# Performance work log

Measured on AMD Instinct MI355X. Metric: run time of the kernel, lower is better.

The kernel has to match this reference:

```python
import jax, jax.numpy as jnp
import numpy as np

MIDC = 128
HEADS = 4
HEADC = MIDC // HEADS
EPS = 1e-5


def _layernorm(x, w, b):
    # Faithful to the custom torch LayerNorm: unbiased std (ddof=1) and (std + eps) in denominator.
    mean = jnp.mean(x, axis=-1, keepdims=True)
    std = jnp.std(x, axis=-1, keepdims=True, ddof=1)
    return w * ((x - mean) / (std + EPS)) + b


def setup_inputs() -> dict:
    key = jax.random.key(0)
    ks = jax.random.split(key, 8)
    B, C, D, H, W = 2, MIDC, 16, 64, 64
    s = 1.0 / np.sqrt(C)
    return {
        "x": jax.random.normal(ks[0], (B, C, D, H, W), dtype=jnp.float32),
        "qkv_w": jax.random.normal(ks[1], (3 * C, C), dtype=jnp.float32) * s,
        "qkv_b": jnp.zeros((3 * C,), dtype=jnp.float32),
        "o1_w": jax.random.normal(ks[2], (C, C), dtype=jnp.float32) * s,
        "o1_b": jnp.zeros((C,), dtype=jnp.float32),
        "o2_w": jax.random.normal(ks[3], (C, C), dtype=jnp.float32) * s,
        "o2_b": jnp.zeros((C,), dtype=jnp.float32),
        "kln_w": jnp.ones((HEADS, 1, HEADC), dtype=jnp.float32),
        "kln_b": jnp.zeros((HEADS, 1, HEADC), dtype=jnp.float32),
        "vln_w": jnp.ones((HEADS, 1, HEADC), dtype=jnp.float32),
        "vln_b": jnp.zeros((HEADS, 1, HEADC), dtype=jnp.float32),
    }


def reference(x, qkv_w, qkv_b, o1_w, o1_b, o2_w, o2_b, kln_w, kln_b, vln_w, vln_b):
    B, C, D, H, W = x.shape
    heads, headc = HEADS, HEADC
    bias = x
    # 1x1x1 Conv3d == pointwise linear over channel dim
    qkv = jnp.einsum('bcdhw,oc->bdhwo', x, qkv_w) + qkv_b          # [B,D,H,W,3C]
    qkv = qkv.reshape(B * D, H * W, heads, 3 * headc)
    qkv = qkv.transpose(0, 2, 1, 3)                                 # [BD,heads,HW,3hc]
    q, k, v = jnp.split(qkv, 3, axis=-1)                            # each [BD,heads,HW,hc]
    k = _layernorm(k, kln_w, kln_b)
    v = _layernorm(v, vln_w, vln_b)
    # linear attention: (K^T V) then Q (K^T V)
    kv = jnp.einsum('bhnc,bhnd->bhcd', k, v) / (H * W)              # [BD,heads,hc,hc]
    v = jnp.einsum('bhnc,bhcd->bhnd', q, kv)                        # [BD,heads,HW,hc]
    v = v.transpose(0, 2, 1, 3).reshape(B, D, H, W, C)
    ret = v.transpose(0, 4, 1, 2, 3) + bias                         # [B,C,D,H,W]
    h = jnp.einsum('bcdhw,oc->bodhw', ret, o1_w) + o1_b[None, :, None, None, None]
    h = jax.nn.gelu(h, approximate=False)
    out = jnp.einsum('bcdhw,oc->bodhw', h, o2_w) + o2_b[None, :, None, None, None]
    return out + bias
```

## Files before the change

### kernel.cpp

```cpp
#include <hip/hip_runtime.h>
#include <cmath>

typedef float  f32x4  __attribute__((ext_vector_type(4)));
typedef __bf16 bf16x8 __attribute__((ext_vector_type(8)));
typedef __bf16 bf16x4 __attribute__((ext_vector_type(4)));
typedef __bf16 bf16x2 __attribute__((ext_vector_type(2)));

#define MFMA16(acc, a, b) (acc) = __builtin_amdgcn_mfma_f32_16x16x32_bf16((a), (b), (acc), 0, 0, 0)


__device__ __forceinline__ int swz(int row, int colByte){ return row*256 + (colByte ^ ((row & 7) << 4)); }
__device__ __forceinline__ int swzP(int row, int colByte){ return row*128 + (colByte ^ ((row & 7) << 4)); }

__device__ __forceinline__ void loadx(float* sx, const float* __restrict__ xb, int t){
  int p = t & 63, cg = t >> 6;
  const float* col = xb + p;
  #pragma unroll
  for (int i = 0; i < 4; ++i)
    #pragma unroll
    for (int j = 0; j < 8; ++j)
      sx[i*8 + j] = col[(cg*8 + i*32 + j) * 65536];
}
__device__ __forceinline__ void writex(const float* sx, char* ldsX, int t){
  int p = t & 63, cg = t >> 6;
  #pragma unroll
  for (int i = 0; i < 4; ++i){
    bf16x8 u;
    #pragma unroll
    for (int j = 0; j < 8; ++j) u[j] = (__bf16)sx[i*8 + j];
    *(bf16x8*)(ldsX + swz(p, cg*16 + i*64)) = u;
  }
}

__global__ __launch_bounds__(256) void wprep(const float* __restrict__ qkv_w,
                                             const float* __restrict__ o1w,
                                             const float* __restrict__ o2w,
                                             __bf16* __restrict__ w16){
  int e = (blockIdx.x * 256 + threadIdx.x) * 4;
  const float* src; int off;
  if (e < 49152)      { src = qkv_w; off = e; }
  else if (e < 65536) { src = o1w;   off = e - 49152; }
  else                { src = o2w;   off = e - 65536; }
  f32x4 v = *(const f32x4*)(src + off);
  bf16x4 o;
  #pragma unroll
  for (int r = 0; r < 4; ++r) o[r] = (__bf16)v[r];
  *(bf16x4*)(w16 + e) = o;
}

__global__ __launch_bounds__(256) void k1_kv(
    const float* __restrict__ x, const __bf16* __restrict__ w16, const float* __restrict__ qkv_b,
    const float* __restrict__ klw, const float* __restrict__ klb,
    const float* __restrict__ vlw, const float* __restrict__ vlb,
    __bf16* __restrict__ part){
  __shared__ char ldsX[16384];
  __shared__ char ksS[4][4096];
  int t = threadIdx.x, lane = t & 63, w = t >> 6, l15 = lane & 15, l4 = lane >> 4;
  int bx = blockIdx.x, bd = bx >> 6, b = bd >> 4, d = bd & 15;
  const float* xb = x + (size_t)b*8388608 + d*4096 + (bx & 63)*64;
  char* ks = ksS[w];
  char* vs = ldsX + w * 4096;

  {
    float sx[32];
    loadx(sx, xb, t);
    writex(sx, ldsX, t);
  }
  __syncthreads();

  bf16x4 pv0[4], pv1[4];
  #pragma unroll
  for (int ph = 0; ph < 2; ++ph){
    int po = 96*w + 32 + 32*ph;
    f32x4 acc[2][4] = {};
    #pragma unroll
    for (int kf = 0; kf < 4; ++kf){
      bf16x8 a0 = *(const bf16x8*)(w16 + (po + l15)*128 + kf*32 + l4*8);
      bf16x8 a1 = *(const bf16x8*)(w16 + (po + 16 + l15)*128 + kf*32 + l4*8);
      bf16x8 bn0 = *(const bf16x8*)(ldsX + swz(l15,      kf*64 + l4*16));
      bf16x8 bn1 = *(const bf16x8*)(ldsX + swz(16 + l15, kf*64 + l4*16));
      bf16x8 bn2 = *(const bf16x8*)(ldsX + swz(32 + l15, kf*64 + l4*16));
      bf16x8 bn3 = *(const bf16x8*)(ldsX + swz(48 + l15, kf*64 + l4*16));
      MFMA16(acc[0][0], a0, bn0); MFMA16(acc[0][1], a0, bn1);
      MFMA16(acc[0][2], a0, bn2); MFMA16(acc[0][3], a0, bn3);
      MFMA16(acc[1][0], a1, bn0); MFMA16(acc[1][1], a1, bn1);
      MFMA16(acc[1][2], a1, bn2); MFMA16(acc[1][3], a1, bn3);
    }
    const float* lwp = (ph ? vlw : klw) + 32*w;
    const float* lbp = (ph ? vlb : klb) + 32*w;
    f32x4 b0  = *(const f32x4*)(qkv_b + po + l4*4);
    f32x4 b1  = *(const f32x4*)(qkv_b + po + 16 + l4*4);
    f32x4 lw0 = *(const f32x4*)(lwp + l4*4), lw1 = *(const f32x4*)(lwp + 16 + l4*4);
    f32x4 lb0 = *(const f32x4*)(lbp + l4*4), lb1 = *(const f32x4*)(lbp + 16 + l4*4);
    #pragma unroll
    for (int n = 0; n < 4; ++n){
      f32x4 v0 = acc[0][n] + b0;
      f32x4 v1 = acc[1][n] + b1;
      float s1 = v0[0]+v0[1]+v0[2]+v0[3] + v1[0]+v1[1]+v1[2]+v1[3];
      float s2 = v0[0]*v0[0]+v0[1]*v0[1]+v0[2]*v0[2]+v0[3]*v0[3]
               + v1[0]*v1[0]+v1[1]*v1[1]+v1[2]*v1[2]+v1[3]*v1[3];
      s1 += __shfl_xor(s1, 16); s2 += __shfl_xor(s2, 16);
      s1 += __shfl_xor(s1, 32); s2 += __shfl_xor(s2, 32);
      float m   = s1 * (1.f/32.f);
      float var = fmaxf((s2 - 32.f*m*m) * (1.f/31.f), 0.f);
      float inv = 1.f / (sqrtf(var) + 1e-5f);
      v0 = (v0 - m) * inv * lw0 + lb0;
      v1 = (v1 - m) * inv * lw1 + lb1;
      if (ph == 0){
        int pB = (16*n + l15) * 2;
        #pragma unroll
        for (int r = 0; r < 4; ++r){
          *(__bf16*)(ks + swzP(l4*4 + r, pB))      = (__bf16)v0[r];
          *(__bf16*)(ks + swzP(16 + l4*4 + r, pB)) = (__bf16)v1[r];
        }
      } else {
        #pragma unroll
        for (int r = 0; r < 4; ++r){ pv0[n][r] = (__bf16)v0[r]; pv1[n][r] = (__bf16)v1[r]; }
      }
    }
  }
  __syncthreads();
  #pragma unroll
  for (int n = 0; n < 4; ++n){
    int pB = (16*n + l15) * 2;
    #pragma unroll
    for (int r = 0; r < 4; ++r){
      *(__bf16*)(vs + swzP(l4*4 + r, pB))      = pv0[n][r];
      *(__bf16*)(vs + swzP(16 + l4*4 + r, pB)) = pv1[n][r];
    }
  }
  f32x4 kv[2][2] = {};
  #pragma unroll
  for (int kf = 0; kf < 2; ++kf){
    bf16x8 av0 = *(const bf16x8*)(vs + swzP(l15,      kf*64 + l4*16));
    bf16x8 av1 = *(const bf16x8*)(vs + swzP(16 + l15, kf*64 + l4*16));
    bf16x8 bk0 = *(const bf16x8*)(ks + swzP(l15,      kf*64 + l4*16));
    bf16x8 bk1 = *(const bf16x8*)(ks + swzP(16 + l15, kf*64 + l4*16));
    MFMA16(kv[0][0], av0, bk0); MFMA16(kv[0][1], av0, bk1);
    MFMA16(kv[1][0], av1, bk0); MFMA16(kv[1][1], av1, bk1);
  }

  __bf16* pb = part + (size_t)bx*4096 + w*1024;
  #pragma unroll
  for (int m = 0; m < 2; ++m)
    #pragma unroll
    for (int n = 0; n < 2; ++n)
      #pragma unroll
      for (int r = 0; r < 4; ++r)
        pb[(16*m + l4*4 + r)*32 + 16*n + l15] = (__bf16)kv[m][n][r];
}

__global__ __launch_bounds__(256) void k15_reduce(const __bf16* __restrict__ part,
                                                  float* __restrict__ kvt){
  int bx = blockIdx.x, t = threadIdx.x;
  int bd = bx >> 3, seg = bx & 7;
  int e = seg * 512 + t * 2;
  float s0 = 0.f, s1 = 0.f;
  #pragma unroll
  for (int sub = 0; sub < 64; ++sub){
    bf16x2 p = *(const bf16x2*)(part + (size_t)(bd * 64 + sub) * 4096 + e);
    s0 += (float)p[0]; s1 += (float)p[1];
  }
  kvt[bd * 4096 + e]     = s0 * (1.f / 4096.f);
  kvt[bd * 4096 + e + 1] = s1 * (1.f / 4096.f);
}

__global__ __launch_bounds__(256, 5) void k2_main(
    const float* __restrict__ x, const __bf16* __restrict__ w16, const float* __restrict__ qkv_b,
    const float* __restrict__ o1b, const float* __restrict__ o2b,
    const float* __restrict__ kvt, float* __restrict__ out){
  __shared__ char lx[16384];
  __shared__ char wk[16384];
  int t = threadIdx.x, lane = t & 63, w = t >> 6, l15 = lane & 15, l4 = lane >> 4;
  int bx = blockIdx.x, bd = bx >> 6, b = bd >> 4, d = bd & 15;
  size_t gofs = (size_t)b*8388608 + d*4096 + (bx & 63)*64;
  const float* xb = x + gofs;
  float* ob = out + gofs;
  const __bf16* w1 = w16 + 49152;
  const __bf16* w2 = w16 + 65536;
  int oo = 32 * w;

  float sx[32];
  loadx(sx, xb, t);
  const float* kvh = kvt + ((size_t)bd*4 + w)*1024;
  f32x4 ql0 = *(const f32x4*)(kvh + l15*32 + l4*8);
  f32x4 qh0 = *(const f32x4*)(kvh + l15*32 + l4*8 + 4);
  f32x4 ql1 = *(const f32x4*)(kvh + (16 + l15)*32 + l4*8);
  f32x4 qh1 = *(const f32x4*)(kvh + (16 + l15)*32 + l4*8 + 4);
  writex(sx, lx, t);
  bf16x8 ka0, ka1;
  #pragma unroll
  for (int j = 0; j < 4; ++j){
    ka0[j] = (__bf16)ql0[j]; ka0[j+4] = (__bf16)qh0[j];
    ka1[j] = (__bf16)ql1[j]; ka1[j+4] = (__bf16)qh1[j];
  }
  __syncthreads();

  {
    bf16x8 A0[4], A1[4];
    #pragma unroll
    for (int kf = 0; kf < 4; ++kf){
      A0[kf] = *(const bf16x8*)(w16 + (96*w + l15)*128 + kf*32 + l4*8);
      A1[kf] = *(const bf16x8*)(w16 + (96*w + 16 + l15)*128 + kf*32 + l4*8);
    }
    f32x4 acc[2][4] = {};
    #pragma unroll
    for (int kf = 0; kf < 4; ++kf){
      bf16x8 bn0 = *(const bf16x8*)(lx + swz(l15,      kf*64 + l4*16));
      bf16x8 bn1 = *(const bf16x8*)(lx + swz(16 + l15, kf*64 + l4*16));
      bf16x8 bn2 = *(const bf16x8*)(lx + swz(32 + l15, kf*64 + l4*16));
      bf16x8 bn3 = *(const bf16x8*)(lx + swz(48 + l15, kf*64 + l4*16));
      MFMA16(acc[0][0], A0[kf], bn0); MFMA16(acc[0][1], A0[kf], bn1);
      MFMA16(acc[0][2], A0[kf], bn2); MFMA16(acc[0][3], A0[kf], bn3);
      MFMA16(acc[1][0], A1[kf], bn0); MFMA16(acc[1][1], A1[kf], bn1);
      MFMA16(acc[1][2], A1[kf], bn2); MFMA16(acc[1][3], A1[kf], bn3);
    }
    #pragma unroll
    for (int m = 0; m < 2; ++m){
      f32x4 qb = *(const f32x4*)(qkv_b + 96*w + 16*m + l4*4);
      int cB = (oo + 16*m + l4*4) * 2;
      #pragma unroll
      for (int n = 0; n < 4; ++n){
        bf16x4 pk;
        #pragma unroll
        for (int r = 0; r < 4; ++r) pk[r] = (__bf16)(acc[m][n][r] + qb[r]);
        *(bf16x4*)(wk + swz(16*n + l15, cB)) = pk;
      }
    }
  }
  {
    f32x4 acc[2][4] = {};
    #pragma unroll
    for (int n = 0; n < 4; ++n){
      bf16x8 bq = *(const bf16x8*)(wk + swz(16*n + l15, oo*2 + l4*16));
      MFMA16(acc[0][n], ka0, bq);
      MFMA16(acc[1][n], ka1, bq);
    }
    #pragma unroll
    for (int m = 0; m < 2; ++m){
      int cB = (oo + 16*m + l4*4) * 2;
      #pragma unroll
      for (int n = 0; n < 4; ++n){
        bf16x4 xv = *(const bf16x4*)(lx + swz(16*n + l15, cB));
        bf16x4 pk;
        #pragma unroll
        for (int r = 0; r < 4; ++r) pk[r] = (__bf16)(acc[m][n][r] + (float)xv[r]);
        *(bf16x4*)(wk + swz(16*n + l15, cB)) = pk;
      }
    }
  }
  __syncthreads();

  {
    bf16x8 A0[4], A1[4];
    #pragma unroll
    for (int kf = 0; kf < 4; ++kf){
      A0[kf] = *(const bf16x8*)(w1 + (oo + l15)*128 + kf*32 + l4*8);
      A1[kf] = *(const bf16x8*)(w1 + (oo + 16 + l15)*128 + kf*32 + l4*8);
    }
    f32x4 acc1[2][4] = {};
    #pragma unroll
    for (int kf = 0; kf < 4; ++kf){
      bf16x8 bn0 = *(const bf16x8*)(wk + swz(l15,      kf*64 + l4*16));
      bf16x8 bn1 = *(const bf16x8*)(wk + swz(16 + l15, kf*64 + l4*16));
      bf16x8 bn2 = *(const bf16x8*)(wk + swz(32 + l15, kf*64 + l4*16));
      bf16x8 bn3 = *(const bf16x8*)(wk + swz(48 + l15, kf*64 + l4*16));
      MFMA16(acc1[0][0], A0[kf], bn0); MFMA16(acc1[0][1], A0[kf], bn1);
      MFMA16(acc1[0][2], A0[kf], bn2); MFMA16(acc1[0][3], A0[kf], bn3);
      MFMA16(acc1[1][0], A1[kf], bn0); MFMA16(acc1[1][1], A1[kf], bn1);
      MFMA16(acc1[1][2], A1[kf], bn2); MFMA16(acc1[1][3], A1[kf], bn3);
    }
    bf16x4 hk[2][4];
    #pragma unroll
    for (int m = 0; m < 2; ++m){
      f32x4 bb = *(const f32x4*)(o1b + oo + 16*m + l4*4);
      #pragma unroll
      for (int n = 0; n < 4; ++n)
        #pragma unroll
        for (int r = 0; r < 4; ++r){
          float v = acc1[m][n][r] + bb[r];
          float z = v * (1.5957691216f + 0.0713548164f * v * v);
          hk[m][n][r] = (__bf16)(v / (1.f + __expf(-z)));
        }
    }
    __syncthreads();
    #pragma unroll
    for (int m = 0; m < 2; ++m){
      int cB = (oo + 16*m + l4*4) * 2;
      #pragma unroll
      for (int n = 0; n < 4; ++n)
        *(bf16x4*)(wk + swz(16*n + l15, cB)) = hk[m][n];
    }
  }
  __syncthreads();

  {
    bf16x8 A0[4], A1[4];
    #pragma unroll
    for (int kf = 0; kf < 4; ++kf){
      A0[kf] = *(const bf16x8*)(w2 + (oo + l15)*128 + kf*32 + l4*8);
      A1[kf] = *(const bf16x8*)(w2 + (oo + 16 + l15)*128 + kf*32 + l4*8);
    }
    f32x4 acc2[2][4] = {};
    #pragma unroll
    for (int kf = 0; kf < 4; ++kf){
      bf16x8 bn0 = *(const bf16x8*)(wk + swz(l15,      kf*64 + l4*16));
      bf16x8 bn1 = *(const bf16x8*)(wk + swz(16 + l15, kf*64 + l4*16));
      bf16x8 bn2 = *(const bf16x8*)(wk + swz(32 + l15, kf*64 + l4*16));
      bf16x8 bn3 = *(const bf16x8*)(wk + swz(48 + l15, kf*64 + l4*16));
      MFMA16(acc2[0][0], A0[kf], bn0); MFMA16(acc2[0][1], A0[kf], bn1);
      MFMA16(acc2[0][2], A0[kf], bn2); MFMA16(acc2[0][3], A0[kf], bn3);
      MFMA16(acc2[1][0], A1[kf], bn0); MFMA16(acc2[1][1], A1[kf], bn1);
      MFMA16(acc2[1][2], A1[kf], bn2); MFMA16(acc2[1][3], A1[kf], bn3);
    }
    #pragma unroll
    for (int m = 0; m < 2; ++m){
      int c0 = oo + 16*m + l4*4;
      f32x4 bb = *(const f32x4*)(o2b + c0);
      #pragma unroll
      for (int n = 0; n < 4; ++n){
        bf16x4 xv = *(const bf16x4*)(lx + swz(16*n + l15, c0*2));
        #pragma unroll
        for (int r = 0; r < 4; ++r)
          ob[(size_t)(c0 + r)*65536 + 16*n + l15] = acc2[m][n][r] + bb[r] + (float)xv[r];
      }
    }
  }
}

extern "C" void kernel_launch(void* const* d_in, const int* in_sizes, int n_in,
                              void* d_out, int out_size, void* d_ws, size_t ws_size,
                              hipStream_t stream){
  const float* x     = (const float*)d_in[0];
  const float* qkv_w = (const float*)d_in[1];
  const float* qkv_b = (const float*)d_in[2];
  const float* o1w   = (const float*)d_in[3];
  const float* o1b   = (const float*)d_in[4];
  const float* o2w   = (const float*)d_in[5];
  const float* o2b   = (const float*)d_in[6];
  const float* klw   = (const float*)d_in[7];
  const float* klb   = (const float*)d_in[8];
  const float* vlw   = (const float*)d_in[9];
  const float* vlb   = (const float*)d_in[10];

  __bf16* part = (__bf16*)d_out;
  float*  kvt  = (float*)d_ws;
  __bf16* w16  = (__bf16*)((char*)d_ws + 524288);

  wprep<<<80, 256, 0, stream>>>(qkv_w, o1w, o2w, w16);
  k1_kv<<<2048, 256, 0, stream>>>(x, w16, qkv_b, klw, klb, vlw, vlb, part);
  k15_reduce<<<256, 256, 0, stream>>>(part, kvt);
  k2_main<<<2048, 256, 0, stream>>>(x, w16, qkv_b, o1b, o2b, kvt, (float*)d_out);
}
```

Measured before the change: 92.00 us.

## Repartition k2_main so each wave owns 16 pixels through QKV, attention and o1

Moves the per-wave split in the fused main kernel from output-channel slices to pixel slices for the q projection, the Q·KV product and the first output conv. Each wave keeps its own 16-pixel activations in a private 4 KB LDS region, which removes two block-wide barriers and the shared staging between stages. Each wave now loads all weight rows from global memory for its MFMAs, where before it loaded only its channel slice. The occupancy hint of 5 in launch_bounds is also dropped, which changes register allocation and could raise register pressure.

```diff
diff --git a/kernel.cpp b/kernel.cpp
--- a/kernel.cpp
+++ b/kernel.cpp
@@ -165,7 +165,7 @@
   kvt[bd * 4096 + e + 1] = s1 * (1.f / 4096.f);
 }
 
-__global__ __launch_bounds__(256, 5) void k2_main(
+__global__ __launch_bounds__(256) void k2_main(
     const float* __restrict__ x, const __bf16* __restrict__ w16, const float* __restrict__ qkv_b,
     const float* __restrict__ o1b, const float* __restrict__ o2b,
     const float* __restrict__ kvt, float* __restrict__ out){
@@ -178,140 +178,113 @@
   float* ob = out + gofs;
   const __bf16* w1 = w16 + 49152;
   const __bf16* w2 = w16 + 65536;
-  int oo = 32 * w;
-
-  float sx[32];
-  loadx(sx, xb, t);
-  const float* kvh = kvt + ((size_t)bd*4 + w)*1024;
-  f32x4 ql0 = *(const f32x4*)(kvh + l15*32 + l4*8);
-  f32x4 qh0 = *(const f32x4*)(kvh + l15*32 + l4*8 + 4);
-  f32x4 ql1 = *(const f32x4*)(kvh + (16 + l15)*32 + l4*8);
-  f32x4 qh1 = *(const f32x4*)(kvh + (16 + l15)*32 + l4*8 + 4);
-  writex(sx, lx, t);
-  bf16x8 ka0, ka1;
-  #pragma unroll
-  for (int j = 0; j < 4; ++j){
-    ka0[j] = (__bf16)ql0[j]; ka0[j+4] = (__bf16)qh0[j];
-    ka1[j] = (__bf16)ql1[j]; ka1[j+4] = (__bf16)qh1[j];
+  char* s = wk + w * 4096;
+
+  {
+    float sx[32];
+    loadx(sx, xb, t);
+    writex(sx, lx, t);
   }
   __syncthreads();
 
   {
-    bf16x8 A0[4], A1[4];
+    f32x4 acc[8] = {};
     #pragma unroll
     for (int kf = 0; kf < 4; ++kf){
-      A0[kf] = *(const bf16x8*)(w16 + (96*w + l15)*128 + kf*32 + l4*8);
-      A1[kf] = *(const bf16x8*)(w16 + (96*w + 16 + l15)*128 + kf*32 + l4*8);
-    }
-    f32x4 acc[2][4] = {};
+      bf16x8 bq = *(const bf16x8*)(lx + swz(w*16 + l15, kf*64 + l4*16));
+      #pragma unroll
+      for (int m = 0; m < 8; ++m){
+        bf16x8 a = *(const bf16x8*)(w16 + (96*(m>>1) + (m&1)*16 + l15)*128 + kf*32 + l4*8);
+        MFMA16(acc[m], a, bq);
+      }
+    }
+    #pragma unroll
+    for (int m = 0; m < 8; ++m){
+      f32x4 qb = *(const f32x4*)(qkv_b + 96*(m>>1) + (m&1)*16 + l4*4);
+      int ch0 = 32*(m>>1) + (m&1)*16 + l4*4;
+      bf16x4 pk;
+      #pragma unroll
+      for (int r = 0; r < 4; ++r) pk[r] = (__bf16)(acc[m][r] + qb[r]);
+      *(bf16x4*)(s + swz(l15, ch0*2)) = pk;
+    }
+  }
+
+  {
+    const float* kvb = kvt + (size_t)bd*4096;
+    #pragma unroll
+    for (int h = 0; h < 4; ++h){
+      const float* kvh = kvb + h*1024;
+      f32x4 ql0 = *(const f32x4*)(kvh + l15*32 + l4*8);
+      f32x4 qh0 = *(const f32x4*)(kvh + l15*32 + l4*8 + 4);
+      f32x4 ql1 = *(const f32x4*)(kvh + (16 + l15)*32 + l4*8);
+      f32x4 qh1 = *(const f32x4*)(kvh + (16 + l15)*32 + l4*8 + 4);
+      bf16x8 ka0, ka1;
+      #pragma unroll
+      for (int j = 0; j < 4; ++j){
+        ka0[j] = (__bf16)ql0[j]; ka0[j+4] = (__bf16)qh0[j];
+        ka1[j] = (__bf16)ql1[j]; ka1[j+4] = (__bf16)qh1[j];
+      }
+      bf16x8 bq = *(const bf16x8*)(s + swz(l15, h*64 + l4*16));
+      f32x4 r0 = {}, r1 = {};
+      MFMA16(r0, ka0, bq);
+      MFMA16(r1, ka1, bq);
+      int ch0 = 32*h + l4*4;
+      bf16x4 xv0 = *(const bf16x4*)(lx + swz(w*16 + l15, ch0*2));
+      bf16x4 xv1 = *(const bf16x4*)(lx + swz(w*16 + l15, (ch0 + 16)*2));
+      bf16x4 p0, p1;
+      #pragma unroll
+      for (int r = 0; r < 4; ++r){
+        p0[r] = (__bf16)(r0[r] + (float)xv0[r]);
+        p1[r] = (__bf16)(r1[r] + (float)xv1[r]);
+      }
+      *(bf16x4*)(s + swz(l15, ch0*2)) = p0;
+      *(bf16x4*)(s + swz(l15, (ch0 + 16)*2)) = p1;
+    }
+  }
+
+  {
+    bf16x8 bn[4];
+    #pragma unroll
+    for (int kf = 0; kf < 4; ++kf)
+      bn[kf] = *(const bf16x8*)(s + swz(l15, kf*64 + l4*16));
+    f32x4 acc[8] = {};
+    #pragma unroll
+    for (int kf = 0; kf < 4; ++kf)
+      #pragma unroll
+      for (int m = 0; m < 8; ++m){
+        bf16x8 a = *(const bf16x8*)(w1 + (16*m + l15)*128 + kf*32 + l4*8);
+        MFMA16(acc[m], a, bn[kf]);
+      }
+    #pragma unroll
+    for (int m = 0; m < 8; ++m){
+      f32x4 bb = *(const f32x4*)(o1b + 16*m + l4*4);
+      bf16x4 pk;
+      #pragma unroll
+      for (int r = 0; r < 4; ++r){
+        float v = acc[m][r] + bb[r];
+        float z = v * (1.5957691216f + 0.0713548164f * v * v);
+        pk[r] = (__bf16)(v / (1.f + __expf(-z)));
+      }
+      *(bf16x4*)(s + swz(l15, (16*m + l4*4)*2)) = pk;
+    }
+  }
+  __syncthreads();
+
+  {
+    int oo = 32 * w;
+    f32x4 acc2[2][4] = {};
     #pragma unroll
     for (int kf = 0; kf < 4; ++kf){
-      bf16x8 bn0 = *(const bf16x8*)(lx + swz(l15,      kf*64 + l4*16));
-      bf16x8 bn1 = *(const bf16x8*)(lx + swz(16 + l15, kf*64 + l4*16));
-      bf16x8 bn2 = *(const bf16x8*)(lx + swz(32 + l15, kf*64 + l4*16));
-      bf16x8 bn3 = *(const bf16x8*)(lx + swz(48 + l15, kf*64 + l4*16));
-      MFMA16(acc[0][0], A0[kf], bn0); MFMA16(acc[0][1], A0[kf], bn1);
-      MFMA16(acc[0][2], A0[kf], bn2); MFMA16(acc[0][3], A0[kf], bn3);
-      MFMA16(acc[1][0], A1[kf], bn0); MFMA16(acc[1][1], A1[kf], bn1);
-      MFMA16(acc[1][2], A1[kf], bn2); MFMA16(acc[1][3], A1[kf], bn3);
-    }
-    #pragma unroll
-    for (int m = 0; m < 2; ++m){
-      f32x4 qb = *(const f32x4*)(qkv_b + 96*w + 16*m + l4*4);
-      int cB = (oo + 16*m + l4*4) * 2;
-      #pragma unroll
-      for (int n = 0; n < 4; ++n){
-        bf16x4 pk;
-        #pragma unroll
-        for (int r = 0; r < 4; ++r) pk[r] = (__bf16)(acc[m][n][r] + qb[r]);
-        *(bf16x4*)(wk + swz(16*n + l15, cB)) = pk;
-      }
-    }
-  }
-  {
-    f32x4 acc[2][4] = {};
-    #pragma unroll
-    for (int n = 0; n < 4; ++n){
-      bf16x8 bq = *(const bf16x8*)(wk + swz(16*n + l15, oo*2 + l4*16));
-      MFMA16(acc[0][n], ka0, bq);
-      MFMA16(acc[1][n], ka1, bq);
-    }
-    #pragma unroll
-    for (int m = 0; m < 2; ++m){
-      int cB = (oo + 16*m + l4*4) * 2;
-      #pragma unroll
-      for (int n = 0; n < 4; ++n){
-        bf16x4 xv = *(const bf16x4*)(lx + swz(16*n + l15, cB));
-        bf16x4 pk;
-        #pragma unroll
-        for (int r = 0; r < 4; ++r) pk[r] = (__bf16)(acc[m][n][r] + (float)xv[r]);
-        *(bf16x4*)(wk + swz(16*n + l15, cB)) = pk;
-      }
-    }
-  }
-  __syncthreads();
-
-  {
-    bf16x8 A0[4], A1[4];
-    #pragma unroll
-    for (int kf = 0; kf < 4; ++kf){
-      A0[kf] = *(const bf16x8*)(w1 + (oo + l15)*128 + kf*32 + l4*8);
-      A1[kf] = *(const bf16x8*)(w1 + (oo + 16 + l15)*128 + kf*32 + l4*8);
-    }
-    f32x4 acc1[2][4] = {};
-    #pragma unroll
-    for (int kf = 0; kf < 4; ++kf){
-      bf16x8 bn0 = *(const bf16x8*)(wk + swz(l15,      kf*64 + l4*16));
-      bf16x8 bn1 = *(const bf16x8*)(wk + swz(16 + l15, kf*64 + l4*16));
-      bf16x8 bn2 = *(const bf16x8*)(wk + swz(32 + l15, kf*64 + l4*16));
-      bf16x8 bn3 = *(const bf16x8*)(wk + swz(48 + l15, kf*64 + l4*16));
-      MFMA16(acc1[0][0], A0[kf], bn0); MFMA16(acc1[0][1], A0[kf], bn1);
-      MFMA16(acc1[0][2], A0[kf], bn2); MFMA16(acc1[0][3], A0[kf], bn3);
-      MFMA16(acc1[1][0], A1[kf], bn0); MFMA16(acc1[1][1], A1[kf], bn1);
-      MFMA16(acc1[1][2], A1[kf], bn2); MFMA16(acc1[1][3], A1[kf], bn3);
-    }
-    bf16x4 hk[2][4];
-    #pragma unroll
-    for (int m = 0; m < 2; ++m){
-      f32x4 bb = *(const f32x4*)(o1b + oo + 16*m + l4*4);
-      #pragma unroll
-      for (int n = 0; n < 4; ++n)
-        #pragma unroll
-        for (int r = 0; r < 4; ++r){
-          float v = acc1[m][n][r] + bb[r];
-          float z = v * (1.5957691216f + 0.0713548164f * v * v);
-          hk[m][n][r] = (__bf16)(v / (1.f + __expf(-z)));
-        }
-    }
-    __syncthreads();
-    #pragma unroll
-    for (int m = 0; m < 2; ++m){
-      int cB = (oo + 16*m + l4*4) * 2;
-      #pragma unroll
-      for (int n = 0; n < 4; ++n)
-        *(bf16x4*)(wk + swz(16*n + l15, cB)) = hk[m][n];
-    }
-  }
-  __syncthreads();
-
-  {
-    bf16x8 A0[4], A1[4];
-    #pragma unroll
-    for (int kf = 0; kf < 4; ++kf){
-      A0[kf] = *(const bf16x8*)(w2 + (oo + l15)*128 + kf*32 + l4*8);
-      A1[kf] = *(const bf16x8*)(w2 + (oo + 16 + l15)*128 + kf*32 + l4*8);
-    }
-    f32x4 acc2[2][4] = {};
-    #pragma unroll
-    for (int kf = 0; kf < 4; ++kf){
-      bf16x8 bn0 = *(const bf16x8*)(wk + swz(l15,      kf*64 + l4*16));
-      bf16x8 bn1 = *(const bf16x8*)(wk + swz(16 + l15, kf*64 + l4*16));
-      bf16x8 bn2 = *(const bf16x8*)(wk + swz(32 + l15, kf*64 + l4*16));
-      bf16x8 bn3 = *(const bf16x8*)(wk + swz(48 + l15, kf*64 + l4*16));
-      MFMA16(acc2[0][0], A0[kf], bn0); MFMA16(acc2[0][1], A0[kf], bn1);
-      MFMA16(acc2[0][2], A0[kf], bn2); MFMA16(acc2[0][3], A0[kf], bn3);
-      MFMA16(acc2[1][0], A1[kf], bn0); MFMA16(acc2[1][1], A1[kf], bn1);
-      MFMA16(acc2[1][2], A1[kf], bn2); MFMA16(acc2[1][3], A1[kf], bn3);
+      bf16x8 a0 = *(const bf16x8*)(w2 + (oo + l15)*128 + kf*32 + l4*8);
+      bf16x8 a1 = *(const bf16x8*)(w2 + (oo + 16 + l15)*128 + kf*32 + l4*8);
+      bf16x8 bn0 = *(const bf16x8*)(wk +        swz(l15, kf*64 + l4*16));
+      bf16x8 bn1 = *(const bf16x8*)(wk + 4096 + swz(l15, kf*64 + l4*16));
+      bf16x8 bn2 = *(const bf16x8*)(wk + 8192 + swz(l15, kf*64 + l4*16));
+      bf16x8 bn3 = *(const bf16x8*)(wk + 12288 + swz(l15, kf*64 + l4*16));
+      MFMA16(acc2[0][0], a0, bn0); MFMA16(acc2[0][1], a0, bn1);
+      MFMA16(acc2[0][2], a0, bn2); MFMA16(acc2[0][3], a0, bn3);
+      MFMA16(acc2[1][0], a1, bn0); MFMA16(acc2[1][1], a1, bn1);
+      MFMA16(acc2[1][2], a1, bn2); MFMA16(acc2[1][3], a1, bn3);
     }
     #pragma unroll
     for (int m = 0; m < 2; ++m){
```

After: 140.0 us. +52.1%, slower.

## Alias shared buffers in main kernel and split k/v projection into halves

Applied to the files above, without the earlier changes.

The main kernel now uses a single 16KB LDS buffer instead of two. The residual x tile is kept in registers, and an extra barrier lets the Q projection overwrite the x tile in place. The W2 fragments are loaded inside the k-loop rather than preloaded, and the launch-bounds occupancy hint is dropped. In the first kernel, the K/V projection plus layernorm is split into two half-width passes to shrink the accumulator footprint. Together these aim to cut LDS and register pressure so more blocks fit per CU, at the cost of an extra synchronization and more register-held residual data.

```diff
diff --git a/kernel.cpp b/kernel.cpp
--- a/kernel.cpp
+++ b/kernel.cpp
@@ -72,50 +72,50 @@
   #pragma unroll
   for (int ph = 0; ph < 2; ++ph){
     int po = 96*w + 32 + 32*ph;
-    f32x4 acc[2][4] = {};
-    #pragma unroll
-    for (int kf = 0; kf < 4; ++kf){
-      bf16x8 a0 = *(const bf16x8*)(w16 + (po + l15)*128 + kf*32 + l4*8);
-      bf16x8 a1 = *(const bf16x8*)(w16 + (po + 16 + l15)*128 + kf*32 + l4*8);
-      bf16x8 bn0 = *(const bf16x8*)(ldsX + swz(l15,      kf*64 + l4*16));
-      bf16x8 bn1 = *(const bf16x8*)(ldsX + swz(16 + l15, kf*64 + l4*16));
-      bf16x8 bn2 = *(const bf16x8*)(ldsX + swz(32 + l15, kf*64 + l4*16));
-      bf16x8 bn3 = *(const bf16x8*)(ldsX + swz(48 + l15, kf*64 + l4*16));
-      MFMA16(acc[0][0], a0, bn0); MFMA16(acc[0][1], a0, bn1);
-      MFMA16(acc[0][2], a0, bn2); MFMA16(acc[0][3], a0, bn3);
-      MFMA16(acc[1][0], a1, bn0); MFMA16(acc[1][1], a1, bn1);
-      MFMA16(acc[1][2], a1, bn2); MFMA16(acc[1][3], a1, bn3);
-    }
-    const float* lwp = (ph ? vlw : klw) + 32*w;
-    const float* lbp = (ph ? vlb : klb) + 32*w;
-    f32x4 b0  = *(const f32x4*)(qkv_b + po + l4*4);
-    f32x4 b1  = *(const f32x4*)(qkv_b + po + 16 + l4*4);
-    f32x4 lw0 = *(const f32x4*)(lwp + l4*4), lw1 = *(const f32x4*)(lwp + 16 + l4*4);
-    f32x4 lb0 = *(const f32x4*)(lbp + l4*4), lb1 = *(const f32x4*)(lbp + 16 + l4*4);
-    #pragma unroll
-    for (int n = 0; n < 4; ++n){
-      f32x4 v0 = acc[0][n] + b0;
-      f32x4 v1 = acc[1][n] + b1;
-      float s1 = v0[0]+v0[1]+v0[2]+v0[3] + v1[0]+v1[1]+v1[2]+v1[3];
-      float s2 = v0[0]*v0[0]+v0[1]*v0[1]+v0[2]*v0[2]+v0[3]*v0[3]
-               + v1[0]*v1[0]+v1[1]*v1[1]+v1[2]*v1[2]+v1[3]*v1[3];
-      s1 += __shfl_xor(s1, 16); s2 += __shfl_xor(s2, 16);
-      s1 += __shfl_xor(s1, 32); s2 += __shfl_xor(s2, 32);
-      float m   = s1 * (1.f/32.f);
-      float var = fmaxf((s2 - 32.f*m*m) * (1.f/31.f), 0.f);
-      float inv = 1.f / (sqrtf(var) + 1e-5f);
-      v0 = (v0 - m) * inv * lw0 + lb0;
-      v1 = (v1 - m) * inv * lw1 + lb1;
-      if (ph == 0){
-        int pB = (16*n + l15) * 2;
-        #pragma unroll
-        for (int r = 0; r < 4; ++r){
-          *(__bf16*)(ks + swzP(l4*4 + r, pB))      = (__bf16)v0[r];
-          *(__bf16*)(ks + swzP(16 + l4*4 + r, pB)) = (__bf16)v1[r];
+    #pragma unroll
+    for (int nh = 0; nh < 2; ++nh){
+      f32x4 acc[2][2] = {};
+      #pragma unroll
+      for (int kf = 0; kf < 4; ++kf){
+        bf16x8 a0 = *(const bf16x8*)(w16 + (po + l15)*128 + kf*32 + l4*8);
+        bf16x8 a1 = *(const bf16x8*)(w16 + (po + 16 + l15)*128 + kf*32 + l4*8);
+        bf16x8 bn0 = *(const bf16x8*)(ldsX + swz(32*nh + l15,      kf*64 + l4*16));
+        bf16x8 bn1 = *(const bf16x8*)(ldsX + swz(32*nh + 16 + l15, kf*64 + l4*16));
+        MFMA16(acc[0][0], a0, bn0); MFMA16(acc[0][1], a0, bn1);
+        MFMA16(acc[1][0], a1, bn0); MFMA16(acc[1][1], a1, bn1);
+      }
+      const float* lwp = (ph ? vlw : klw) + 32*w;
+      const float* lbp = (ph ? vlb : klb) + 32*w;
+      f32x4 b0  = *(const f32x4*)(qkv_b + po + l4*4);
+      f32x4 b1  = *(const f32x4*)(qkv_b + po + 16 + l4*4);
+      f32x4 lw0 = *(const f32x4*)(lwp + l4*4), lw1 = *(const f32x4*)(lwp + 16 + l4*4);
+      f32x4 lb0 = *(const f32x4*)(lbp + l4*4), lb1 = *(const f32x4*)(lbp + 16 + l4*4);
+      #pragma unroll
+      for (int nn = 0; nn < 2; ++nn){
+        int n = 2*nh + nn;
+        f32x4 v0 = acc[0][nn] + b0;
+        f32x4 v1 = acc[1][nn] + b1;
+        float s1 = v0[0]+v0[1]+v0[2]+v0[3] + v1[0]+v1[1]+v1[2]+v1[3];
+        float s2 = v0[0]*v0[0]+v0[1]*v0[1]+v0[2]*v0[2]+v0[3]*v0[3]
+                 + v1[0]*v1[0]+v1[1]*v1[1]+v1[2]*v1[2]+v1[3]*v1[3];
+        s1 += __shfl_xor(s1, 16); s2 += __shfl_xor(s2, 16);
+        s1 += __shfl_xor(s1, 32); s2 += __shfl_xor(s2, 32);
+        float m   = s1 * (1.f/32.f);
+        float var = fmaxf((s2 - 32.f*m*m) * (1.f/31.f), 0.f);
+        float inv = 1.f / (sqrtf(var) + 1e-5f);
+        v0 = (v0 - m) * inv * lw0 + lb0;
+        v1 = (v1 - m) * inv * lw1 + lb1;
+        if (ph == 0){
+          int pB = (16*n + l15) * 2;
+          #pragma unroll
+          for (int r = 0; r < 4; ++r){
+            *(__bf16*)(ks + swzP(l4*4 + r, pB))      = (__bf16)v0[r];
+            *(__bf16*)(ks + swzP(16 + l4*4 + r, pB)) = (__bf16)v1[r];
+          }
+        } else {
+          #pragma unroll
+          for (int r = 0; r < 4; ++r){ pv0[n][r] = (__bf16)v0[r]; pv1[n][r] = (__bf16)v1[r]; }
         }
-      } else {
-        #pragma unroll
-        for (int r = 0; r < 4; ++r){ pv0[n][r] = (__bf16)v0[r]; pv1[n][r] = (__bf16)v1[r]; }
       }
     }
   }
@@ -165,12 +165,11 @@
   kvt[bd * 4096 + e + 1] = s1 * (1.f / 4096.f);
 }
 
-__global__ __launch_bounds__(256, 5) void k2_main(
+__global__ __launch_bounds__(256) void k2_main(
     const float* __restrict__ x, const __bf16* __restrict__ w16, const float* __restrict__ qkv_b,
     const float* __restrict__ o1b, const float* __restrict__ o2b,
     const float* __restrict__ kvt, float* __restrict__ out){
-  __shared__ char lx[16384];
-  __shared__ char wk[16384];
+  __shared__ char L[16384];
   int t = threadIdx.x, lane = t & 63, w = t >> 6, l15 = lane & 15, l4 = lane >> 4;
   int bx = blockIdx.x, bd = bx >> 6, b = bd >> 4, d = bd & 15;
   size_t gofs = (size_t)b*8388608 + d*4096 + (bx & 63)*64;
@@ -180,14 +179,16 @@
   const __bf16* w2 = w16 + 65536;
   int oo = 32 * w;
 
-  float sx[32];
-  loadx(sx, xb, t);
+  {
+    float sx[32];
+    loadx(sx, xb, t);
+    writex(sx, L, t);
+  }
   const float* kvh = kvt + ((size_t)bd*4 + w)*1024;
   f32x4 ql0 = *(const f32x4*)(kvh + l15*32 + l4*8);
   f32x4 qh0 = *(const f32x4*)(kvh + l15*32 + l4*8 + 4);
   f32x4 ql1 = *(const f32x4*)(kvh + (16 + l15)*32 + l4*8);
   f32x4 qh1 = *(const f32x4*)(kvh + (16 + l15)*32 + l4*8 + 4);
-  writex(sx, lx, t);
   bf16x8 ka0, ka1;
   #pragma unroll
   for (int j = 0; j < 4; ++j){
@@ -196,6 +197,14 @@
   }
   __syncthreads();
 
+  bf16x4 xr[2][4];
+  #pragma unroll
+  for (int m = 0; m < 2; ++m)
+    #pragma unroll
+    for (int n = 0; n < 4; ++n)
+      xr[m][n] = *(const bf16x4*)(L + swz(16*n + l15, (oo + 16*m + l4*4)*2));
+
+  bf16x4 qk[2][4];
   {
     bf16x8 A0[4], A1[4];
     #pragma unroll
@@ -206,10 +215,10 @@
     f32x4 acc[2][4] = {};
     #pragma unroll
     for (int kf = 0; kf < 4; ++kf){
-      bf16x8 bn0 = *(const bf16x8*)(lx + swz(l15,      kf*64 + l4*16));
-      bf16x8 bn1 = *(const bf16x8*)(lx + swz(16 + l15, kf*64 + l4*16));
-      bf16x8 bn2 = *(const bf16x8*)(lx + swz(32 + l15, kf*64 + l4*16));
-      bf16x8 bn3 = *(const bf16x8*)(lx + swz(48 + l15, kf*64 + l4*16));
+      bf16x8 bn0 = *(const bf16x8*)(L + swz(l15,      kf*64 + l4*16));
+      bf16x8 bn1 = *(const bf16x8*)(L + swz(16 + l15, kf*64 + l4*16));
+      bf16x8 bn2 = *(const bf16x8*)(L + swz(32 + l15, kf*64 + l4*16));
+      bf16x8 bn3 = *(const bf16x8*)(L + swz(48 + l15, kf*64 + l4*16));
       MFMA16(acc[0][0], A0[kf], bn0); MFMA16(acc[0][1], A0[kf], bn1);
       MFMA16(acc[0][2], A0[kf], bn2); MFMA16(acc[0][3], A0[kf], bn3);
       MFMA16(acc[1][0], A1[kf], bn0); MFMA16(acc[1][1], A1[kf], bn1);
@@ -218,34 +227,38 @@
     #pragma unroll
     for (int m = 0; m < 2; ++m){
       f32x4 qb = *(const f32x4*)(qkv_b + 96*w + 16*m + l4*4);
+      #pragma unroll
+      for (int n = 0; n < 4; ++n)
+        #pragma unroll
+        for (int r = 0; r < 4; ++r) qk[m][n][r] = (__bf16)(acc[m][n][r] + qb[r]);
+    }
+  }
+  __syncthreads();
+
+  #pragma unroll
+  for (int m = 0; m < 2; ++m){
+    int cB = (oo + 16*m + l4*4) * 2;
+    #pragma unroll
+    for (int n = 0; n < 4; ++n)
+      *(bf16x4*)(L + swz(16*n + l15, cB)) = qk[m][n];
+  }
+  {
+    f32x4 acc[2][4] = {};
+    #pragma unroll
+    for (int n = 0; n < 4; ++n){
+      bf16x8 bq = *(const bf16x8*)(L + swz(16*n + l15, oo*2 + l4*16));
+      MFMA16(acc[0][n], ka0, bq);
+      MFMA16(acc[1][n], ka1, bq);
+    }
+    #pragma unroll
+    for (int m = 0; m < 2; ++m){
       int cB = (oo + 16*m + l4*4) * 2;
       #pragma unroll
       for (int n = 0; n < 4; ++n){
         bf16x4 pk;
         #pragma unroll
-        for (int r = 0; r < 4; ++r) pk[r] = (__bf16)(acc[m][n][r] + qb[r]);
-        *(bf16x4*)(wk + swz(16*n + l15, cB)) = pk;
-      }
-    }
-  }
-  {
-    f32x4 acc[2][4] = {};
-    #pragma unroll
-    for (int n = 0; n < 4; ++n){
-      bf16x8 bq = *(const bf16x8*)(wk + swz(16*n + l15, oo*2 + l4*16));
-      MFMA16(acc[0][n], ka0, bq);
-      MFMA16(acc[1][n], ka1, bq);
-    }
-    #pragma unroll
-    for (int m = 0; m < 2; ++m){
-      int cB = (oo + 16*m + l4*4) * 2;
-      #pragma unroll
-      for (int n = 0; n < 4; ++n){
-        bf16x4 xv = *(const bf16x4*)(lx + swz(16*n + l15, cB));
-        bf16x4 pk;
-        #pragma unroll
-        for (int r = 0; r < 4; ++r) pk[r] = (__bf16)(acc[m][n][r] + (float)xv[r]);
-        *(bf16x4*)(wk + swz(16*n + l15, cB)) = pk;
+        for (int r = 0; r < 4; ++r) pk[r] = (__bf16)(acc[m][n][r] + (float)xr[m][n][r]);
+        *(bf16x4*)(L + swz(16*n + l15, cB)) = pk;
       }
     }
   }
@@ -261,10 +274,10 @@
     f32x4 acc1[2][4] = {};
     #pragma unroll
     for (int kf = 0; kf < 4; ++kf){
-      bf16x8 bn0 = *(const bf16x8*)(wk + swz(l15,      kf*64 + l4*16));
-      bf16x8 bn1 = *(const bf16x8*)(wk + swz(16 + l15, kf*64 + l4*16));
-      bf16x8 bn2 = *(const bf16x8*)(wk + swz(32 + l15, kf*64 + l4*16));
-      bf16x8 bn3 = *(const bf16x8*)(wk + swz(48 + l15, kf*64 + l4*16));
+      bf16x8 bn0 = *(const bf16x8*)(L + swz(l15,      kf*64 + l4*16));
+      bf16x8 bn1 = *(const bf16x8*)(L + swz(16 + l15, kf*64 + l4*16));
+      bf16x8 bn2 = *(const bf16x8*)(L + swz(32 + l15, kf*64 + l4*16));
+      bf16x8 bn3 = *(const bf16x8*)(L + swz(48 + l15, kf*64 + l4*16));
       MFMA16(acc1[0][0], A0[kf], bn0); MFMA16(acc1[0][1], A0[kf], bn1);
       MFMA16(acc1[0][2], A0[kf], bn2); MFMA16(acc1[0][3], A0[kf], bn3);
       MFMA16(acc1[1][0], A1[kf], bn0); MFMA16(acc1[1][1], A1[kf], bn1);
@@ -289,41 +302,35 @@
       int cB = (oo + 16*m + l4*4) * 2;
       #pragma unroll
       for (int n = 0; n < 4; ++n)
-        *(bf16x4*)(wk + swz(16*n + l15, cB)) = hk[m][n];
-    }
-  }
-  __syncthreads();
-
-  {
-    bf16x8 A0[4], A1[4];
-    #pragma unroll
-    for (int kf = 0; kf < 4; ++kf){
-      A0[kf] = *(const bf16x8*)(w2 + (oo + l15)*128 + kf*32 + l4*8);
-      A1[kf] = *(const bf16x8*)(w2 + (oo + 16 + l15)*128 + kf*32 + l4*8);
-    }
+        *(bf16x4*)(L + swz(16*n + l15, cB)) = hk[m][n];
+    }
+  }
+  __syncthreads();
+
+  {
     f32x4 acc2[2][4] = {};
     #pragma unroll
     for (int kf = 0; kf < 4; ++kf){
-      bf16x8 bn0 = *(const bf16x8*)(wk + swz(l15,      kf*64 + l4*16));
-      bf16x8 bn1 = *(const bf16x8*)(wk + swz(16 + l15, kf*64 + l4*16));
-      bf16x8 bn2 = *(const bf16x8*)(wk + swz(32 + l15, kf*64 + l4*16));
-      bf16x8 bn3 = *(const bf16x8*)(wk + swz(48 + l15, kf*64 + l4*16));
-      MFMA16(acc2[0][0], A0[kf], bn0); MFMA16(acc2[0][1], A0[kf], bn1);
-      MFMA16(acc2[0][2], A0[kf], bn2); MFMA16(acc2[0][3], A0[kf], bn3);
-      MFMA16(acc2[1][0], A1[kf], bn0); MFMA16(acc2[1][1], A1[kf], bn1);
-      MFMA16(acc2[1][2], A1[kf], bn2); MFMA16(acc2[1][3], A1[kf], bn3);
+      bf16x8 a0 = *(const bf16x8*)(w2 + (oo + l15)*128 + kf*32 + l4*8);
+      bf16x8 a1 = *(const bf16x8*)(w2 + (oo + 16 + l15)*128 + kf*32 + l4*8);
+      bf16x8 bn0 = *(const bf16x8*)(L + swz(l15,      kf*64 + l4*16));
+      bf16x8 bn1 = *(const bf16x8*)(L + swz(16 + l15, kf*64 + l4*16));
+      bf16x8 bn2 = *(const bf16x8*)(L + swz(32 + l15, kf*64 + l4*16));
+      bf16x8 bn3 = *(const bf16x8*)(L + swz(48 + l15, kf*64 + l4*16));
+      MFMA16(acc2[0][0], a0, bn0); MFMA16(acc2[0][1], a0, bn1);
+      MFMA16(acc2[0][2], a0, bn2); MFMA16(acc2[0][3], a0, bn3);
+      MFMA16(acc2[1][0], a1, bn0); MFMA16(acc2[1][1], a1, bn1);
+      MFMA16(acc2[1][2], a1, bn2); MFMA16(acc2[1][3], a1, bn3);
     }
     #pragma unroll
     for (int m = 0; m < 2; ++m){
       int c0 = oo + 16*m + l4*4;
       f32x4 bb = *(const f32x4*)(o2b + c0);
       #pragma unroll
-      for (int n = 0; n < 4; ++n){
-        bf16x4 xv = *(const bf16x4*)(lx + swz(16*n + l15, c0*2));
+      for (int n = 0; n < 4; ++n)
         #pragma unroll
         for (int r = 0; r < 4; ++r)
-          ob[(size_t)(c0 + r)*65536 + 16*n + l15] = acc2[m][n][r] + bb[r] + (float)xv[r];
-      }
+          ob[(size_t)(c0 + r)*65536 + 16*n + l15] = acc2[m][n][r] + bb[r] + (float)xr[m][n][r];
     }
   }
 }
```

New measurement: 99.28 us. 1.08x slower.

## Fold KV matrix and residual into per-slice effective Q weight matrix

Applied to the files above, without the earlier changes.

Replaces the KV reduce kernel with one that also multiplies the reduced per-head KV matrix into the Q projection weights, adds identity for the residual, and computes an effective bias. The main kernel then does a single GEMM with this per-slice effective weight instead of a Q projection, a KV MFMA stage and a residual add. This removes one MFMA stage plus LDS round trips per tile. In exchange it adds a small serial weight-folding kernel and per-slice bf16 weights read from global memory. The launch-bounds occupancy hint of 5 is also dropped. Folding the identity into bf16 weights may change rounding of the residual path.

```diff
diff --git a/kernel.cpp b/kernel.cpp
--- a/kernel.cpp
+++ b/kernel.cpp
@@ -4,7 +4,6 @@
 typedef float  f32x4  __attribute__((ext_vector_type(4)));
 typedef __bf16 bf16x8 __attribute__((ext_vector_type(8)));
 typedef __bf16 bf16x4 __attribute__((ext_vector_type(4)));
-typedef __bf16 bf16x2 __attribute__((ext_vector_type(2)));
 
 #define MFMA16(acc, a, b) (acc) = __builtin_amdgcn_mfma_f32_16x16x32_bf16((a), (b), (acc), 0, 0, 0)
 
@@ -150,25 +149,53 @@
         pb[(16*m + l4*4 + r)*32 + 16*n + l15] = (__bf16)kv[m][n][r];
 }
 
-__global__ __launch_bounds__(256) void k15_reduce(const __bf16* __restrict__ part,
-                                                  float* __restrict__ kvt){
-  int bx = blockIdx.x, t = threadIdx.x;
-  int bd = bx >> 3, seg = bx & 7;
-  int e = seg * 512 + t * 2;
-  float s0 = 0.f, s1 = 0.f;
-  #pragma unroll
-  for (int sub = 0; sub < 64; ++sub){
-    bf16x2 p = *(const bf16x2*)(part + (size_t)(bd * 64 + sub) * 4096 + e);
-    s0 += (float)p[0]; s1 += (float)p[1];
-  }
-  kvt[bd * 4096 + e]     = s0 * (1.f / 4096.f);
-  kvt[bd * 4096 + e + 1] = s1 * (1.f / 4096.f);
-}
-
-__global__ __launch_bounds__(256, 5) void k2_main(
-    const float* __restrict__ x, const __bf16* __restrict__ w16, const float* __restrict__ qkv_b,
+__global__ __launch_bounds__(256) void kweff(
+    const __bf16* __restrict__ part, const __bf16* __restrict__ w16,
+    const float* __restrict__ qkv_b,
+    __bf16* __restrict__ weff, float* __restrict__ beff){
+  __shared__ float kvsh[1024];
+  int t = threadIdx.x, bx = blockIdx.x;
+  int bd = bx >> 2, h = bx & 3;
+
+  {
+    f32x4 s = {0.f, 0.f, 0.f, 0.f};
+    const __bf16* pb = part + (size_t)bd*64*4096 + h*1024 + t*4;
+    for (int sub = 0; sub < 64; ++sub){
+      bf16x4 p = *(const bf16x4*)(pb + (size_t)sub*4096);
+      #pragma unroll
+      for (int r = 0; r < 4; ++r) s[r] += (float)p[r];
+    }
+    #pragma unroll
+    for (int r = 0; r < 4; ++r) kvsh[t*4 + r] = s[r] * (1.f/4096.f);
+  }
+  __syncthreads();
+
+  int j = t & 127, half = t >> 7;
+  float wq[32];
+  #pragma unroll
+  for (int c = 0; c < 32; ++c) wq[c] = (float)w16[(96*h + c)*128 + j];
+  #pragma unroll
+  for (int dq = 0; dq < 16; ++dq){
+    int dd = half*16 + dq;
+    float s = 0.f;
+    #pragma unroll
+    for (int c = 0; c < 32; ++c) s += kvsh[dd*32 + c] * wq[c];
+    if (32*h + dd == j) s += 1.f;
+    weff[(size_t)bd*16384 + (32*h + dd)*128 + j] = (__bf16)s;
+  }
+  if (t < 32){
+    float s = 0.f;
+    #pragma unroll
+    for (int c = 0; c < 32; ++c) s += qkv_b[96*h + c] * kvsh[t*32 + c];
+    beff[bd*128 + 32*h + t] = s;
+  }
+}
+
+__global__ __launch_bounds__(256) void k2_main(
+    const float* __restrict__ x, const __bf16* __restrict__ w16,
+    const __bf16* __restrict__ weff, const float* __restrict__ beff,
     const float* __restrict__ o1b, const float* __restrict__ o2b,
-    const float* __restrict__ kvt, float* __restrict__ out){
+    float* __restrict__ out){
   __shared__ char lx[16384];
   __shared__ char wk[16384];
   int t = threadIdx.x, lane = t & 63, w = t >> 6, l15 = lane & 15, l4 = lane >> 4;
@@ -178,21 +205,13 @@
   float* ob = out + gofs;
   const __bf16* w1 = w16 + 49152;
   const __bf16* w2 = w16 + 65536;
+  const __bf16* we = weff + (size_t)bd*16384;
   int oo = 32 * w;
 
-  float sx[32];
-  loadx(sx, xb, t);
-  const float* kvh = kvt + ((size_t)bd*4 + w)*1024;
-  f32x4 ql0 = *(const f32x4*)(kvh + l15*32 + l4*8);
-  f32x4 qh0 = *(const f32x4*)(kvh + l15*32 + l4*8 + 4);
-  f32x4 ql1 = *(const f32x4*)(kvh + (16 + l15)*32 + l4*8);
-  f32x4 qh1 = *(const f32x4*)(kvh + (16 + l15)*32 + l4*8 + 4);
-  writex(sx, lx, t);
-  bf16x8 ka0, ka1;
-  #pragma unroll
-  for (int j = 0; j < 4; ++j){
-    ka0[j] = (__bf16)ql0[j]; ka0[j+4] = (__bf16)qh0[j];
-    ka1[j] = (__bf16)ql1[j]; ka1[j+4] = (__bf16)qh1[j];
+  {
+    float sx[32];
+    loadx(sx, xb, t);
+    writex(sx, lx, t);
   }
   __syncthreads();
 
@@ -200,8 +219,8 @@
     bf16x8 A0[4], A1[4];
     #pragma unroll
     for (int kf = 0; kf < 4; ++kf){
-      A0[kf] = *(const bf16x8*)(w16 + (96*w + l15)*128 + kf*32 + l4*8);
-      A1[kf] = *(const bf16x8*)(w16 + (96*w + 16 + l15)*128 + kf*32 + l4*8);
+      A0[kf] = *(const bf16x8*)(we + (oo + l15)*128 + kf*32 + l4*8);
+      A1[kf] = *(const bf16x8*)(we + (oo + 16 + l15)*128 + kf*32 + l4*8);
     }
     f32x4 acc[2][4] = {};
     #pragma unroll
@@ -217,34 +236,13 @@
     }
     #pragma unroll
     for (int m = 0; m < 2; ++m){
-      f32x4 qb = *(const f32x4*)(qkv_b + 96*w + 16*m + l4*4);
+      f32x4 bb = *(const f32x4*)(beff + bd*128 + oo + 16*m + l4*4);
       int cB = (oo + 16*m + l4*4) * 2;
       #pragma unroll
       for (int n = 0; n < 4; ++n){
         bf16x4 pk;
         #pragma unroll
-        for (int r = 0; r < 4; ++r) pk[r] = (__bf16)(acc[m][n][r] + qb[r]);
-        *(bf16x4*)(wk + swz(16*n + l15, cB)) = pk;
-      }
-    }
-  }
-  {
-    f32x4 acc[2][4] = {};
-    #pragma unroll
-    for (int n = 0; n < 4; ++n){
-      bf16x8 bq = *(const bf16x8*)(wk + swz(16*n + l15, oo*2 + l4*16));
-      MFMA16(acc[0][n], ka0, bq);
-      MFMA16(acc[1][n], ka1, bq);
-    }
-    #pragma unroll
-    for (int m = 0; m < 2; ++m){
-      int cB = (oo + 16*m + l4*4) * 2;
-      #pragma unroll
-      for (int n = 0; n < 4; ++n){
-        bf16x4 xv = *(const bf16x4*)(lx + swz(16*n + l15, cB));
-        bf16x4 pk;
-        #pragma unroll
-        for (int r = 0; r < 4; ++r) pk[r] = (__bf16)(acc[m][n][r] + (float)xv[r]);
+        for (int r = 0; r < 4; ++r) pk[r] = (__bf16)(acc[m][n][r] + bb[r]);
         *(bf16x4*)(wk + swz(16*n + l15, cB)) = pk;
       }
     }
@@ -344,11 +342,12 @@
   const float* vlb   = (const float*)d_in[10];
 
   __bf16* part = (__bf16*)d_out;
-  float*  kvt  = (float*)d_ws;
-  __bf16* w16  = (__bf16*)((char*)d_ws + 524288);
+  __bf16* weff = (__bf16*)d_ws;
+  float*  beff = (float*)((char*)d_ws + 1048576);
+  __bf16* w16  = (__bf16*)((char*)d_ws + 1064960);
 
   wprep<<<80, 256, 0, stream>>>(qkv_w, o1w, o2w, w16);
   k1_kv<<<2048, 256, 0, stream>>>(x, w16, qkv_b, klw, klb, vlw, vlb, part);
-  k15_reduce<<<256, 256, 0, stream>>>(part, kvt);
-  k2_main<<<2048, 256, 0, stream>>>(x, w16, qkv_b, o1b, o2b, kvt, (float*)d_out);
-}
+  kweff<<<128, 256, 0, stream>>>(part, w16, qkv_b, weff, beff);
+  k2_main<<<2048, 256, 0, stream>>>(x, w16, weff, beff, o1b, o2b, (float*)d_out);
+}
```

Result: no change. 91.97 us (-0.0%).
